# Optimization experiments

Measured on AMD Instinct MI355X. Metric: run time of the kernel, lower is better.

Reference implementation:

```python
import jax, jax.numpy as jnp
import numpy as np

B, CIN, COUT, K, H, W = 8, 512, 512, 3, 64, 64
SCALE = 1.0 / np.sqrt(CIN * K * K).astype(np.float32)  # conv.scale
LRELU_SCALE = 1.4142135623730951  # sqrt(2), FusedLeakyReLU scale


def setup_inputs() -> dict:
    key = jax.random.key(0)
    ks = jax.random.split(key, 6)
    return {
        "x": jax.random.normal(ks[0], (B, CIN, H, W), jnp.float32),
        "style": jax.random.normal(ks[1], (B, CIN), jnp.float32),
        "noise": jax.random.normal(ks[2], (1, 1, H, W), jnp.float32),
        "weight": jax.random.normal(ks[3], (COUT, CIN, K, K), jnp.float32),
        "bias": jnp.zeros((COUT,), jnp.float32),
        "noise_strength": jax.random.uniform(ks[4], (1,), jnp.float32),
    }


def reference(x, style, noise, weight, bias, noise_strength):
    # Modulate: scale * weight * style  -> [B, Cout, Cin, K, K]
    w = SCALE * weight[None] * style[:, None, :, None, None]
    # Demodulate per (batch, out_channel)
    demod = jax.lax.rsqrt(jnp.sum(w * w, axis=(2, 3, 4)) + 1e-8)
    w = w * demod[:, :, None, None, None]
    # Per-sample conv (grouped-conv trick in torch) via vmap over batch
    pad = K // 2
    def conv_one(xi, wi):  # xi: [Cin,H,W], wi: [Cout,Cin,K,K]
        return jax.lax.conv_general_dilated(
            xi[None], wi, window_strides=(1, 1),
            padding=[(pad, pad), (pad, pad)],
            dimension_numbers=("NCHW", "OIHW", "NCHW"))[0]
    out = jax.vmap(conv_one)(x, w)  # [B, Cout, H, W]
    # NoiseInjection: out + strength * noise (noise broadcast over B, C)
    out = out + noise_strength[0] * noise
    # FusedLeakyReLU: leaky_relu(out + bias, 0.2) * sqrt(2)
    y = out + bias[None, :, None, None]
    return jnp.where(y >= 0, y, 0.2 * y) * LRELU_SCALE
```

## Files before the change

kernel.cpp:

```cpp
#include <hip/hip_runtime.h>
#include <hip/hip_bf16.h>

typedef __attribute__((ext_vector_type(8))) short s16x8;
typedef __attribute__((ext_vector_type(16))) float f32x16;

#define MOD_SCALE 0.014731391274719739f

__device__ __forceinline__ void gload_lds16(const void* g, void* l) {
    __builtin_amdgcn_global_load_lds(
        (const __attribute__((address_space(1))) unsigned int*)g,
        (__attribute__((address_space(3))) unsigned int*)l, 16, 0, 0);
}

__device__ __forceinline__ void sync_drain() {
    __builtin_amdgcn_s_waitcnt(0);
    __syncthreads();
}

__global__ __launch_bounds__(256) void k_prep(const float* __restrict__ x,
                                              const float* __restrict__ style,
                                              const float* __restrict__ weight,
                                              __hip_bfloat16* __restrict__ xs,
                                              __hip_bfloat16* __restrict__ wb,
                                              float* __restrict__ dem) {
    __shared__ __align__(16) char sm[16896];
    const int t = threadIdx.x;
    const int bid = blockIdx.x;

    if (bid < 520) {
        const int idx = bid * 256 + t;
        const int b = idx / 16640;
        const int r2 = idx - b * 16640;
        const int pair = r2 >> 6;
        const int ciq = r2 & 63;
        int pr, pc;
        if (pair < 66)       { pr = 0;          pc = pair; }
        else if (pair < 132) { pr = 65;         pc = pair - 66; }
        else if (pair < 196) { pr = pair - 131; pc = 0; }
        else                 { pr = pair - 195; pc = 65; }
        uint4* d = (uint4*)(xs + (((size_t)b * 66 + pr) * 66 + pc) * 512) + ciq;
        *d = make_uint4(0u, 0u, 0u, 0u);
    } else if (bid < 2568) {
        const int r = bid - 520;
        const int cig = r & 3, h = (r >> 2) & 63, b = r >> 8;
        const int ci0 = cig * 128;
        __hip_bfloat16 (*tile)[130] = (__hip_bfloat16(*)[130])sm;
        const int wl = t & 63, cl4 = t >> 6;
        for (int rr = 0; rr < 32; ++rr) {
            int c = rr * 4 + cl4;
            float v = x[(((size_t)b * 512 + ci0 + c) * 64 + h) * 64 + wl];
            float s = style[b * 512 + ci0 + c];
            tile[wl][c] = __float2bfloat16(v * s * MOD_SCALE);
        }
        __syncthreads();
        const int w4 = t >> 6;
        const int cp = (t & 63) * 2;
        for (int rr = 0; rr < 16; ++rr) {
            int w = rr * 4 + w4;
            unsigned v = *(const unsigned*)(&tile[w][cp]);
            *(unsigned*)(&xs[(((size_t)b * 66 + h + 1) * 66 + (w + 1)) * 512 +
                             ci0 + cp]) = v;
        }
    } else if (bid < 3592) {
        const int r = bid - 2568;
        float* lds = (float*)sm;
        const int p0 = r * 256;
        const float* src = weight + (size_t)p0 * 9;
#pragma unroll
        for (int k = 0; k < 9; ++k) lds[k * 256 + t] = src[k * 256 + t];
        __syncthreads();
#pragma unroll
        for (int tap = 0; tap < 9; ++tap)
            wb[(size_t)tap * 262144 + p0 + t] = __float2bfloat16(lds[t * 9 + tap]);
    } else {
        const int co = bid - 3592;
        float* s2 = (float*)sm;
        for (int i = t; i < 4096; i += 256) { float v = style[i]; s2[i] = v * v; }
        __syncthreads();
        const float4* wp = (const float4*)(weight + (size_t)co * 4608);
        float acc[8] = {0.f, 0.f, 0.f, 0.f, 0.f, 0.f, 0.f, 0.f};
        for (int j = t; j < 1152; j += 256) {
            float4 v = wp[j];
            float w2[4] = {v.x * v.x, v.y * v.y, v.z * v.z, v.w * v.w};
            int base = j * 4;
#pragma unroll
            for (int e = 0; e < 4; ++e) {
                int ci = (base + e) / 9;
                float ww = w2[e];
#pragma unroll
                for (int bb = 0; bb < 8; ++bb) acc[bb] += ww * s2[bb * 512 + ci];
            }
        }
#pragma unroll
        for (int bb = 0; bb < 8; ++bb)
            for (int off = 32; off > 0; off >>= 1)
                acc[bb] += __shfl_down(acc[bb], off);
        float* red = (float*)(sm + 16384);
        const int wv = t >> 6, lane = t & 63;
        if (lane == 0) {
#pragma unroll
            for (int bb = 0; bb < 8; ++bb) red[wv * 8 + bb] = acc[bb];
        }
        __syncthreads();
        if (t < 8) {
            float s = red[t] + red[8 + t] + red[16 + t] + red[24 + t];
            const float S2 = MOD_SCALE * MOD_SCALE;
            dem[t * 512 + co] = rsqrtf(S2 * s + 1e-8f);
        }
    }
}

__global__ __launch_bounds__(256, 2) void k_conv(
    const __hip_bfloat16* __restrict__ xs,
    const __hip_bfloat16* __restrict__ wb,
    const float* __restrict__ demod,
    const float* __restrict__ noise,
    const float* __restrict__ bias,
    const float* __restrict__ nstr,
    float* __restrict__ out) {
    __shared__ __align__(16) char Xl[25344];
    __shared__ __align__(16) char Wl[2][8192];

    const int t = threadIdx.x;
    const int bi = blockIdx.x;
    const int spat = bi & 127;
    const int b = spat >> 4;
    const int h0 = (spat & 15) << 2;
    const int co0 = (bi >> 7) << 7;
    const int lane = t & 63;
    const int wv = t >> 6;
    const int wm = wv & 1, wn = wv >> 1;
    const int el = lane & 31;
    const int hk = lane >> 5;

    f32x16 acc[2][4];
#pragma unroll
    for (int i = 0; i < 2; ++i)
#pragma unroll
        for (int j = 0; j < 4; ++j)
#pragma unroll
            for (int k = 0; k < 16; ++k) acc[i][j][k] = 0.f;

    const char* xsb = (const char*)xs + (size_t)b * 66 * 66 * 1024;
    const char* xsrc[7];
#pragma unroll
    for (int i = 0; i < 6; ++i) {
        int g = i * 256 + t;
        int e = g >> 2, s = g & 3;
        int gc = (s - (e >> 2)) & 3;
        int row = e / 66, col = e - row * 66;
        xsrc[i] = xsb + (size_t)((h0 + row) * 66 + col) * 1024 + gc * 16;
    }
    {
        int g = 1536 + t;
        int e = g >> 2, s = g & 3;
        int gc = (s - (e >> 2)) & 3;
        int row = e / 66, col = e - row * 66;
        xsrc[6] = xsb + (size_t)((h0 + row) * 66 + col) * 1024 + gc * 16;
    }
    const char* wsrc[2];
#pragma unroll
    for (int i = 0; i < 2; ++i) {
        int g = i * 256 + t;
        int e = g >> 2, s = g & 3;
        int gc = (s - (e >> 2)) & 3;
        wsrc[i] = (const char*)wb + (size_t)(co0 + e) * 1024 + gc * 16;
    }
    const int wvoff = wv << 10;

#pragma unroll
    for (int i = 0; i < 6; ++i) gload_lds16(xsrc[i], Xl + i * 4096 + wvoff);
    if (t < 48) gload_lds16(xsrc[6], Xl + 24576);
#pragma unroll
    for (int i = 0; i < 2; ++i)
        gload_lds16(wsrc[i], Wl[0] + i * 4096 + wvoff);
    sync_drain();

    int g = 0;
    for (int cb = 0; cb < 16; ++cb) {
        const int cboff = cb * 64;
#pragma unroll
        for (int tap = 0; tap < 9; ++tap, ++g) {
            if (tap < 8) {
                char* Wn = Wl[(g + 1) & 1] + wvoff;
#pragma unroll
                for (int i = 0; i < 2; ++i)
                    gload_lds16(wsrc[i] + (size_t)(tap + 1) * 524288 + cboff,
                                Wn + i * 4096);
            } else if (cb < 15) {
                char* Wn = Wl[(g + 1) & 1] + wvoff;
#pragma unroll
                for (int i = 0; i < 2; ++i)
                    gload_lds16(wsrc[i] + cboff + 64, Wn + i * 4096);
            }
            const int dh = tap / 3, dw = tap % 3;
            const char* Wb = Wl[g & 1];
#pragma unroll
            for (int ks = 0; ks < 2; ++ks) {
                const int c = 2 * ks + hk;
                s16x8 af[2], bfr[4];
#pragma unroll
                for (int mi = 0; mi < 2; ++mi) {
                    int e = wm * 64 + mi * 32 + el;
                    af[mi] = *(const s16x8*)(Wb + e * 64 +
                                             (((c + (e >> 2)) & 3) << 4));
                }
#pragma unroll
                for (int ni = 0; ni < 4; ++ni) {
                    int e = (2 * wn + (ni >> 1) + dh) * 66 + dw +
                            (ni & 1) * 32 + el;
                    bfr[ni] = *(const s16x8*)(Xl + e * 64 +
                                              (((c + (e >> 2)) & 3) << 4));
                }
#pragma unroll
                for (int mi = 0; mi < 2; ++mi)
#pragma unroll
                    for (int ni = 0; ni < 4; ++ni)
                        acc[mi][ni] = __builtin_amdgcn_mfma_f32_32x32x16_bf16(
                            af[mi], bfr[ni], acc[mi][ni], 0, 0, 0);
            }
            sync_drain();
        }
        if (cb < 15) {
#pragma unroll
            for (int i = 0; i < 6; ++i)
                gload_lds16(xsrc[i] + cboff + 64, Xl + i * 4096 + wvoff);
            if (t < 48) gload_lds16(xsrc[6] + cboff + 64, Xl + 24576);
            sync_drain();
        }
    }

    const float nsv = nstr[0];
    const float LR = 1.4142135623730951f;
#pragma unroll
    for (int mi = 0; mi < 2; ++mi) {
        float dm[16], bs[16];
#pragma unroll
        for (int rg = 0; rg < 16; ++rg) {
            int co = co0 + wm * 64 + mi * 32 + (rg & 3) + 8 * (rg >> 2) + 4 * hk;
            dm[rg] = demod[b * 512 + co];
            bs[rg] = bias[co];
        }
#pragma unroll
        for (int ni = 0; ni < 4; ++ni) {
            int h = h0 + 2 * wn + (ni >> 1);
            int w = (ni & 1) * 32 + el;
            float nz = nsv * noise[h * 64 + w];
#pragma unroll
            for (int rg = 0; rg < 16; ++rg) {
                int co = co0 + wm * 64 + mi * 32 + (rg & 3) + 8 * (rg >> 2) +
                         4 * hk;
                float v = acc[mi][ni][rg] * dm[rg] + nz + bs[rg];
                v = (v >= 0.f ? v : 0.2f * v) * LR;
                out[(((size_t)b * 512 + co) * 64 + h) * 64 + w] = v;
            }
        }
    }
}

extern "C" void kernel_launch(void* const* d_in, const int* in_sizes, int n_in,
                              void* d_out, int out_size, void* d_ws, size_t ws_size,
                              hipStream_t stream) {
    const float* x      = (const float*)d_in[0];
    const float* style  = (const float*)d_in[1];
    const float* noise  = (const float*)d_in[2];
    const float* weight = (const float*)d_in[3];
    const float* bias   = (const float*)d_in[4];
    const float* nstr   = (const float*)d_in[5];
    float* out = (float*)d_out;

    char* ws = (char*)d_ws;
    __hip_bfloat16* xs = (__hip_bfloat16*)ws;
    __hip_bfloat16* wb = (__hip_bfloat16*)(ws + 35684352);
    float* demod = (float*)(ws + 35684352 + 4718592);

    k_prep<<<4104, 256, 0, stream>>>(x, style, weight, xs, wb, demod);
    k_conv<<<512, 256, 0, stream>>>(xs, wb, demod, noise, bias, nstr, out);
}
```

Before: 262.7 us.

## Triple-buffer weight tiles and wait on partial vmcnt between taps

```diff
diff --git a/kernel.cpp b/kernel.cpp
--- a/kernel.cpp
+++ b/kernel.cpp
@@ -15,6 +15,13 @@
 __device__ __forceinline__ void sync_drain() {
     __builtin_amdgcn_s_waitcnt(0);
     __syncthreads();
+}
+
+__device__ __forceinline__ void wait2_barrier() {
+    asm volatile("s_waitcnt vmcnt(2)" ::: "memory");
+    __builtin_amdgcn_sched_barrier(0);
+    __builtin_amdgcn_s_barrier();
+    __builtin_amdgcn_sched_barrier(0);
 }
 
 __global__ __launch_bounds__(256) void k_prep(const float* __restrict__ x,
@@ -119,7 +126,7 @@
     const float* __restrict__ nstr,
     float* __restrict__ out) {
     __shared__ __align__(16) char Xl[25344];
-    __shared__ __align__(16) char Wl[2][8192];
+    __shared__ __align__(16) char Wl[3][8192];
 
     const int t = threadIdx.x;
     const int bi = blockIdx.x;
@@ -174,27 +181,36 @@
 #pragma unroll
     for (int i = 0; i < 2; ++i)
         gload_lds16(wsrc[i], Wl[0] + i * 4096 + wvoff);
+#pragma unroll
+    for (int i = 0; i < 2; ++i)
+        gload_lds16(wsrc[i] + 524288, Wl[1] + i * 4096 + wvoff);
     sync_drain();
 
-    int g = 0;
-    for (int cb = 0; cb < 16; ++cb) {
-        const int cboff = cb * 64;
-#pragma unroll
-        for (int tap = 0; tap < 9; ++tap, ++g) {
-            if (tap < 8) {
-                char* Wn = Wl[(g + 1) & 1] + wvoff;
+    int cboff = 0;
+    for (int cb = 0; cb < 16; ++cb, cboff += 64) {
+        const int ncboff = (cb < 15) ? cboff + 64 : cboff;
+#pragma unroll
+        for (int tap = 0; tap < 9; ++tap) {
+            {
+                char* Wn;
+                size_t woff;
+                if (tap < 7) {
+                    Wn = Wl[(tap + 2) % 3];
+                    woff = (size_t)(tap + 2) * 524288 + cboff;
+                } else if (tap == 7) {
+                    Wn = Wl[0];
+                    woff = (size_t)ncboff;
+                } else {
+                    Wn = Wl[1];
+                    woff = 524288 + (size_t)ncboff;
+                }
+                Wn += wvoff;
 #pragma unroll
                 for (int i = 0; i < 2; ++i)
-                    gload_lds16(wsrc[i] + (size_t)(tap + 1) * 524288 + cboff,
-                                Wn + i * 4096);
-            } else if (cb < 15) {
-                char* Wn = Wl[(g + 1) & 1] + wvoff;
-#pragma unroll
-                for (int i = 0; i < 2; ++i)
-                    gload_lds16(wsrc[i] + cboff + 64, Wn + i * 4096);
+                    gload_lds16(wsrc[i] + woff, Wn + i * 4096);
             }
             const int dh = tap / 3, dw = tap % 3;
-            const char* Wb = Wl[g & 1];
+            const char* Wb = Wl[tap % 3];
 #pragma unroll
             for (int ks = 0; ks < 2; ++ks) {
                 const int c = 2 * ks + hk;
@@ -219,7 +235,8 @@
                         acc[mi][ni] = __builtin_amdgcn_mfma_f32_32x32x16_bf16(
                             af[mi], bfr[ni], acc[mi][ni], 0, 0, 0);
             }
-            sync_drain();
+            if (tap < 8) wait2_barrier();
+            else         sync_drain();
         }
         if (cb < 15) {
 #pragma unroll
```

Result: faster. 254.5 us (-3.1%).

## Load weights directly into registers and double-buffer input tile in LDS

Applied to the files above, without the earlier changes.

```diff
diff --git a/kernel.cpp b/kernel.cpp
--- a/kernel.cpp
+++ b/kernel.cpp
@@ -69,9 +69,19 @@
 #pragma unroll
         for (int k = 0; k < 9; ++k) lds[k * 256 + t] = src[k * 256 + t];
         __syncthreads();
-#pragma unroll
-        for (int tap = 0; tap < 9; ++tap)
-            wb[(size_t)tap * 262144 + p0 + t] = __float2bfloat16(lds[t * 9 + tap]);
+        const int co = r >> 1;
+        const int cb0 = (r & 1) * 8;
+        for (int ch = t; ch < 288; ch += 256) {
+            const int tap = ch >> 5;
+            const int cbl = (ch >> 2) & 7;
+            const int c = ch & 3;
+            union { uint4 u; __hip_bfloat16 h[8]; } pk;
+#pragma unroll
+            for (int j = 0; j < 8; ++j)
+                pk.h[j] = __float2bfloat16(lds[(cbl * 32 + c * 8 + j) * 9 + tap]);
+            *(uint4*)(wb + ((size_t)(tap * 64 + (cb0 + cbl) * 4 + c) * 4096 +
+                            co * 8)) = pk.u;
+        }
     } else {
         const int co = bid - 3592;
         float* s2 = (float*)sm;
@@ -118,8 +128,7 @@
     const float* __restrict__ bias,
     const float* __restrict__ nstr,
     float* __restrict__ out) {
-    __shared__ __align__(16) char Xl[25344];
-    __shared__ __align__(16) char Wl[2][8192];
+    __shared__ __align__(16) char Xl[2][25344];
 
     const int t = threadIdx.x;
     const int bi = blockIdx.x;
@@ -158,58 +167,59 @@
         int row = e / 66, col = e - row * 66;
         xsrc[6] = xsb + (size_t)((h0 + row) * 66 + col) * 1024 + gc * 16;
     }
-    const char* wsrc[2];
-#pragma unroll
-    for (int i = 0; i < 2; ++i) {
-        int g = i * 256 + t;
-        int e = g >> 2, s = g & 3;
-        int gc = (s - (e >> 2)) & 3;
-        wsrc[i] = (const char*)wb + (size_t)(co0 + e) * 1024 + gc * 16;
-    }
     const int wvoff = wv << 10;
 
-#pragma unroll
-    for (int i = 0; i < 6; ++i) gload_lds16(xsrc[i], Xl + i * 4096 + wvoff);
-    if (t < 48) gload_lds16(xsrc[6], Xl + 24576);
-#pragma unroll
-    for (int i = 0; i < 2; ++i)
-        gload_lds16(wsrc[i], Wl[0] + i * 4096 + wvoff);
+    const char* wlane = (const char*)wb +
+                        ((size_t)(co0 + wm * 64 + el) * 8 + (size_t)hk * 4096) * 2;
+
+#pragma unroll
+    for (int i = 0; i < 6; ++i) gload_lds16(xsrc[i], Xl[0] + i * 4096 + wvoff);
+    if (t < 48) gload_lds16(xsrc[6], Xl[0] + 24576);
+    s16x8 wc[2][2];
+#pragma unroll
+    for (int ks = 0; ks < 2; ++ks)
+#pragma unroll
+        for (int mi = 0; mi < 2; ++mi)
+            wc[ks][mi] = *(const s16x8*)(wlane + ks * 16384 + mi * 512);
     sync_drain();
 
-    int g = 0;
     for (int cb = 0; cb < 16; ++cb) {
-        const int cboff = cb * 64;
-#pragma unroll
-        for (int tap = 0; tap < 9; ++tap, ++g) {
-            if (tap < 8) {
-                char* Wn = Wl[(g + 1) & 1] + wvoff;
-#pragma unroll
-                for (int i = 0; i < 2; ++i)
-                    gload_lds16(wsrc[i] + (size_t)(tap + 1) * 524288 + cboff,
-                                Wn + i * 4096);
-            } else if (cb < 15) {
-                char* Wn = Wl[(g + 1) & 1] + wvoff;
-#pragma unroll
-                for (int i = 0; i < 2; ++i)
-                    gload_lds16(wsrc[i] + cboff + 64, Wn + i * 4096);
+        const char* Xr = Xl[cb & 1];
+        if (cb < 15) {
+            char* Xn = Xl[(cb & 1) ^ 1];
+            const int cbo = (cb + 1) * 64;
+#pragma unroll
+            for (int i = 0; i < 6; ++i)
+                gload_lds16(xsrc[i] + cbo, Xn + i * 4096 + wvoff);
+            if (t < 48) gload_lds16(xsrc[6] + cbo, Xn + 24576);
+        }
+        const char* wcb = wlane + (size_t)cb * 32768;
+
+#pragma unroll
+        for (int tap = 0; tap < 9; ++tap) {
+            s16x8 wnx[2][2];
+            {
+                const size_t noff =
+                    (tap < 8) ? (size_t)(tap + 1) * 524288
+                              : (cb < 15 ? (size_t)32768
+                                         : (size_t)0);
+#pragma unroll
+                for (int ks = 0; ks < 2; ++ks)
+#pragma unroll
+                    for (int mi = 0; mi < 2; ++mi)
+                        wnx[ks][mi] = *(const s16x8*)(wcb + noff +
+                                                      ks * 16384 + mi * 512);
             }
             const int dh = tap / 3, dw = tap % 3;
-            const char* Wb = Wl[g & 1];
 #pragma unroll
             for (int ks = 0; ks < 2; ++ks) {
                 const int c = 2 * ks + hk;
-                s16x8 af[2], bfr[4];
-#pragma unroll
-                for (int mi = 0; mi < 2; ++mi) {
-                    int e = wm * 64 + mi * 32 + el;
-                    af[mi] = *(const s16x8*)(Wb + e * 64 +
-                                             (((c + (e >> 2)) & 3) << 4));
-                }
+                s16x8 bfr[4];
 #pragma unroll
                 for (int ni = 0; ni < 4; ++ni) {
                     int e = (2 * wn + (ni >> 1) + dh) * 66 + dw +
                             (ni & 1) * 32 + el;
-                    bfr[ni] = *(const s16x8*)(Xl + e * 64 +
+                    bfr[ni] = *(const s16x8*)(Xr + e * 64 +
                                               (((c + (e >> 2)) & 3) << 4));
                 }
 #pragma unroll
@@ -217,17 +227,15 @@
 #pragma unroll
                     for (int ni = 0; ni < 4; ++ni)
                         acc[mi][ni] = __builtin_amdgcn_mfma_f32_32x32x16_bf16(
-                            af[mi], bfr[ni], acc[mi][ni], 0, 0, 0);
-            }
-            sync_drain();
-        }
-        if (cb < 15) {
-#pragma unroll
-            for (int i = 0; i < 6; ++i)
-                gload_lds16(xsrc[i] + cboff + 64, Xl + i * 4096 + wvoff);
-            if (t < 48) gload_lds16(xsrc[6] + cboff + 64, Xl + 24576);
-            sync_drain();
-        }
+                            wc[ks][mi], bfr[ni], acc[mi][ni], 0, 0, 0);
+            }
+#pragma unroll
+            for (int ks = 0; ks < 2; ++ks)
+#pragma unroll
+                for (int mi = 0; mi < 2; ++mi)
+                    wc[ks][mi] = wnx[ks][mi];
+        }
+        sync_drain();
     }
 
     const float nsv = nstr[0];
```

Result: slower. 357.3 us (+36.0%).
